# Performance work log

Hardware: AMD Instinct MI355X
Metric: run time of the kernel (lower is better)

## Reference

```python
import jax, jax.numpy as jnp
import numpy as np

DIM = 2048
MEM = 64
EPS = 1e-5


def setup_inputs() -> dict:
    key = jax.random.key(0)
    ks = jax.random.split(key, 6)
    x = jax.random.normal(ks[0], (8, 4096, DIM), dtype=jnp.float32)
    memory_slots = jax.random.normal(ks[1], (MEM, DIM), dtype=jnp.float32) * 0.02
    # memory_gate: Linear(dim -> memory_size)
    Wg = jax.random.normal(ks[2], (DIM, MEM), dtype=jnp.float32) / np.sqrt(DIM)
    bg = jnp.zeros((MEM,), dtype=jnp.float32)
    # memory_update: Linear(2*dim -> dim)
    Wu = jax.random.normal(ks[3], (2 * DIM, DIM), dtype=jnp.float32) / np.sqrt(2 * DIM)
    bu = jnp.zeros((DIM,), dtype=jnp.float32)
    gamma = jnp.ones((DIM,), dtype=jnp.float32)
    beta = jnp.zeros((DIM,), dtype=jnp.float32)
    return {"x": x, "memory_slots": memory_slots, "Wg": Wg, "bg": bg,
            "Wu": Wu, "bu": bu, "gamma": gamma, "beta": beta}


def _layer_norm(h, gamma, beta):
    mu = jnp.mean(h, axis=-1, keepdims=True)
    var = jnp.mean(jnp.square(h - mu), axis=-1, keepdims=True)
    return (h - mu) * jax.lax.rsqrt(var + EPS) * gamma + beta


def reference(x, memory_slots, Wg, bg, Wu, bu, gamma, beta):
    # gates: [B, S, M]
    memory_gates = jax.nn.sigmoid(jnp.einsum('bsd,dm->bsm', x, Wg) + bg)
    # retrieval: [B, S, D]
    memory_retrieved = jnp.einsum('bsm,md->bsd', memory_gates, memory_slots)
    combined = jnp.concatenate([x, memory_retrieved], axis=-1)  # [B, S, 2D]
    memory_enhanced = jnp.einsum('bse,ed->bsd', combined, Wu) + bu
    return _layer_norm(memory_enhanced, gamma, beta)
```

## Files before the change

### kernel.cpp

```cpp
#include <hip/hip_runtime.h>
#include <hip/hip_bf16.h>

typedef __bf16 bf16x8 __attribute__((ext_vector_type(8)));
typedef float f32x4 __attribute__((ext_vector_type(4)));
typedef float f32x16 __attribute__((ext_vector_type(16)));
typedef unsigned short u16;
typedef u16 u16x8 __attribute__((ext_vector_type(8)));

#define DIM 2048
#define MEM 64
#define KC 2112
#define MTOK 32768
#define BK 32
#define NT (KC/BK)

__device__ __forceinline__ u16 f2bf(float f) {
  union { float f; unsigned u; } v; v.f = f;
  unsigned r = v.u + 0x7FFF + ((v.u >> 16) & 1);
  return (u16)(r >> 16);
}
__device__ __forceinline__ float bf2f(u16 u) {
  union { unsigned u; float f; } v; v.u = ((unsigned)u) << 16; return v.f;
}

#define GLDS16(g, l) __builtin_amdgcn_global_load_lds( \
    (const __attribute__((address_space(1))) void*)(g), \
    (__attribute__((address_space(3))) void*)(l), 16, 0, 0)

__global__ __launch_bounds__(256) void prep_wu1(const float* __restrict__ Wu,
                                                u16* __restrict__ WcatT) {
  __shared__ float tile[64][65];
  int bk = blockIdx.x & 31;
  int bn = blockIdx.x >> 5;
  int tx = threadIdx.x & 63, g = threadIdx.x >> 6;
#pragma unroll
  for (int i = 0; i < 16; ++i)
    tile[g + i*4][tx] = Wu[(size_t)(bk*64 + g + i*4)*DIM + bn*64 + tx];
  __syncthreads();
#pragma unroll
  for (int i = 0; i < 16; ++i) {
    int n = bn*64 + g + i*4;
    WcatT[(size_t)n*KC + bk*64 + tx] = f2bf(tile[tx][g + i*4]);
  }
}

__global__ __launch_bounds__(256) void prep_m2a(const float* __restrict__ ms,
                                                const float* __restrict__ Wu,
                                                float* __restrict__ M2p) {
  int n  = blockIdx.x*256 + threadIdx.x;
  int mg = blockIdx.y;
  int kc = blockIdx.z;
  const float* w2 = Wu + (size_t)DIM*DIM + n;
  const float* m0 = ms + (size_t)(mg*4+0)*DIM;
  const float* m1 = ms + (size_t)(mg*4+1)*DIM;
  const float* m2 = ms + (size_t)(mg*4+2)*DIM;
  const float* m3 = ms + (size_t)(mg*4+3)*DIM;
  float a0=0.f, a1=0.f, a2=0.f, a3=0.f;
  int d0 = kc*256;
  for (int d = d0; d < d0+256; ++d) {
    float w = w2[(size_t)d*DIM];
    a0 += m0[d]*w; a1 += m1[d]*w; a2 += m2[d]*w; a3 += m3[d]*w;
  }
  M2p[((size_t)kc*64 + mg*4 + 0)*2048 + n] = a0;
  M2p[((size_t)kc*64 + mg*4 + 1)*2048 + n] = a1;
  M2p[((size_t)kc*64 + mg*4 + 2)*2048 + n] = a2;
  M2p[((size_t)kc*64 + mg*4 + 3)*2048 + n] = a3;
}

__global__ __launch_bounds__(256) void prep_m2b(const float* __restrict__ M2p,
                                                u16* __restrict__ WcatT) {
  int i = blockIdx.x*256 + threadIdx.x;
  float s = 0.f;
#pragma unroll
  for (int kc = 0; kc < 8; ++kc) s += M2p[(size_t)kc*131072 + i];
  int m = i >> 11, n = i & 2047;
  WcatT[(size_t)n*KC + DIM + m] = f2bf(s);
}

__global__ __launch_bounds__(256) void prep_wg(const float* __restrict__ Wg,
                                               u16* __restrict__ WgT) {
  __shared__ float tile[64][65];
  int k0 = blockIdx.x * 64;
  int tx = threadIdx.x & 63, g = threadIdx.x >> 6;
#pragma unroll
  for (int i = 0; i < 16; ++i)
    tile[g + i*4][tx] = Wg[(size_t)(k0 + g + i*4)*MEM + tx];
  __syncthreads();
#pragma unroll
  for (int i = 0; i < 16; ++i) {
    int m = g + i*4;
    WgT[(size_t)m*DIM + k0 + tx] = f2bf(tile[tx][m]);
  }
}

__global__ __launch_bounds__(256) void conv_gates(const float* __restrict__ x,
                                                  const u16* __restrict__ WgT,
                                                  const float* __restrict__ bg,
                                                  u16* __restrict__ Acat) {
  __shared__ u16 As[64*32];
  __shared__ u16 Bs[64*32];
  const int brow = blockIdx.x;
  const int tid = threadIdx.x;
  const int w = tid >> 6, l = tid & 63;
  const int wm = w >> 1, wn = w & 1;
  const int lrow = l & 15, lk = l >> 4;

  const int r  = tid >> 2;
  const int cb = (tid & 3) * 8;
  const float* xp = x + (size_t)(brow*64 + r)*DIM + cb;
  u16* aout = Acat + (size_t)(brow*64 + r)*KC + cb;

  f32x4 acc[2][2] = {};
  const bf16x8* Al = reinterpret_cast<const bf16x8*>(As);
  const bf16x8* Bl = reinterpret_cast<const bf16x8*>(Bs);
  const int abase = (wm*32 + lrow)*4 + lk;
  const int bbase = (wn*32 + lrow)*4 + lk;

  float4 v0 = *reinterpret_cast<const float4*>(xp);
  float4 v1 = *reinterpret_cast<const float4*>(xp + 4);

  for (int k0 = 0; k0 < DIM; k0 += 32) {
    const u16* bgp = WgT + (size_t)(tid>>2)*DIM + k0 + (tid&3)*8;
    GLDS16(bgp, ((u16*)Bs) + tid*8);
    u16x8 o;
    o[0]=f2bf(v0.x); o[1]=f2bf(v0.y); o[2]=f2bf(v0.z); o[3]=f2bf(v0.w);
    o[4]=f2bf(v1.x); o[5]=f2bf(v1.y); o[6]=f2bf(v1.z); o[7]=f2bf(v1.w);
    const bool more = (k0 + 32 < DIM);
    if (more) {
      v0 = *reinterpret_cast<const float4*>(xp + k0 + 32);
      v1 = *reinterpret_cast<const float4*>(xp + k0 + 36);
    }
    __builtin_amdgcn_s_barrier();
    *reinterpret_cast<u16x8*>(As + tid*8) = o;
    *reinterpret_cast<u16x8*>(aout + k0) = o;
    if (more) { asm volatile("s_waitcnt vmcnt(3) lgkmcnt(0)" ::: "memory"); }
    else      { asm volatile("s_waitcnt vmcnt(1) lgkmcnt(0)" ::: "memory"); }
    __builtin_amdgcn_sched_barrier(0);
    __builtin_amdgcn_s_barrier();
    bf16x8 a0v = Al[abase], a1v = Al[abase + 64];
    bf16x8 b0v = Bl[bbase], b1v = Bl[bbase + 64];
    acc[0][0] = __builtin_amdgcn_mfma_f32_16x16x32_bf16(a0v, b0v, acc[0][0], 0, 0, 0);
    acc[0][1] = __builtin_amdgcn_mfma_f32_16x16x32_bf16(a0v, b1v, acc[0][1], 0, 0, 0);
    acc[1][0] = __builtin_amdgcn_mfma_f32_16x16x32_bf16(a1v, b0v, acc[1][0], 0, 0, 0);
    acc[1][1] = __builtin_amdgcn_mfma_f32_16x16x32_bf16(a1v, b1v, acc[1][1], 0, 0, 0);
  }

#pragma unroll
  for (int fn = 0; fn < 2; ++fn) {
    int c = wn*32 + fn*16 + lrow;
    float b = bg[c];
#pragma unroll
    for (int fm = 0; fm < 2; ++fm)
#pragma unroll
      for (int rg = 0; rg < 4; ++rg) {
        int t = brow*64 + wm*32 + fm*16 + lk*4 + rg;
        float logit = acc[fm][fn][rg] + b;
        float gv = 1.0f / (1.0f + __expf(-logit));
        Acat[(size_t)t*KC + DIM + c] = f2bf(gv);
      }
  }
}

__global__ __launch_bounds__(512, 2) void gemm_main8(const u16* __restrict__ A,
                                                     const u16* __restrict__ Bt,
                                                     const float* __restrict__ bu,
                                                     float* __restrict__ Hf,
                                                     u16* __restrict__ Hb) {
  __shared__ u16 AsB[4*8192];
  __shared__ u16 BsB[4*8192];

  const int bid = blockIdx.x;
  const int wg  = (bid & 7) * (int)(gridDim.x >> 3) + (bid >> 3);
  const int brow = wg >> 3;
  const int bcol = wg & 7;
  const int tid = threadIdx.x;
  const int w = tid >> 6, l = tid & 63;
  const int wm = w >> 2, wn = w & 3;
  const int l31 = l & 31, lr5 = l >> 5;

  const int xor5  = ((tid >> 5) & 1) << 5;
  const int kelem = (((tid & 3) * 16) ^ xor5) >> 1;
  const int rowst = tid >> 2;
  const u16* Asrc0 = A  + (size_t)(brow*256 + rowst)*KC + kelem;
  const u16* Asrc1 = A  + (size_t)(brow*256 + 128 + rowst)*KC + kelem;
  const u16* Bsrc0 = Bt + (size_t)(bcol*256 + rowst)*KC + kelem;
  const u16* Bsrc1 = Bt + (size_t)(bcol*256 + 128 + rowst)*KC + kelem;
  const int p0 = tid*16, p1 = 8192 + tid*16;
  char* AsC = (char*)AsB;
  char* BsC = (char*)BsB;

  int aoff[4][2], boff[2][2];
#pragma unroll
  for (int rf = 0; rf < 4; ++rf)
#pragma unroll
    for (int ks = 0; ks < 2; ++ks) {
      int row = wm*128 + rf*32 + l31;
      int lg  = row*64 + ks*32 + lr5*16;
      aoff[rf][ks] = lg ^ (((row >> 3) & 1) << 5);
    }
#pragma unroll
  for (int cf = 0; cf < 2; ++cf)
#pragma unroll
    for (int ks = 0; ks < 2; ++ks) {
      int row = wn*64 + cf*32 + l31;
      int lg  = row*64 + ks*32 + lr5*16;
      boff[cf][ks] = lg ^ (((row >> 3) & 1) << 5);
    }

  f32x16 acc[4][2] = {};

#define STAGE_A(kt) { const int bb_ = ((kt)&3)*16384; \
    GLDS16(Asrc0 + (size_t)(kt)*BK, AsC + bb_ + p0); \
    GLDS16(Asrc1 + (size_t)(kt)*BK, AsC + bb_ + p1); }
#define STAGE_B(kt) { const int bb_ = ((kt)&3)*16384; \
    GLDS16(Bsrc0 + (size_t)(kt)*BK, BsC + bb_ + p0); \
    GLDS16(Bsrc1 + (size_t)(kt)*BK, BsC + bb_ + p1); }
#define MFMA32(av, bv, c) __builtin_amdgcn_mfma_f32_32x32x16_bf16(av, bv, c, 0, 0, 0)

  STAGE_A(0); STAGE_B(0);
  STAGE_A(1); STAGE_B(1);
  STAGE_A(2); STAGE_B(2);
  asm volatile("s_waitcnt vmcnt(8)" ::: "memory");
  __builtin_amdgcn_sched_barrier(0);
  __builtin_amdgcn_s_barrier();
  __builtin_amdgcn_sched_barrier(0);

#pragma unroll 1
  for (int t = 0; t < NT; ++t) {
    const char* Ab = AsC + (t & 3) * 16384;
    const char* Bb = BsC + (t & 3) * 16384;

    bf16x8 a0 = *(const bf16x8*)(Ab + aoff[0][0]);
    bf16x8 a1 = *(const bf16x8*)(Ab + aoff[1][0]);
    bf16x8 a2 = *(const bf16x8*)(Ab + aoff[2][0]);
    bf16x8 a3 = *(const bf16x8*)(Ab + aoff[3][0]);
    bf16x8 b0 = *(const bf16x8*)(Bb + boff[0][0]);
    bf16x8 b1 = *(const bf16x8*)(Bb + boff[1][0]);
    if (t + 3 < NT) STAGE_A(t + 3);
    __builtin_amdgcn_s_setprio(1);
    acc[0][0] = MFMA32(a0, b0, acc[0][0]);
    acc[0][1] = MFMA32(a0, b1, acc[0][1]);
    acc[1][0] = MFMA32(a1, b0, acc[1][0]);
    acc[1][1] = MFMA32(a1, b1, acc[1][1]);
    acc[2][0] = MFMA32(a2, b0, acc[2][0]);
    acc[2][1] = MFMA32(a2, b1, acc[2][1]);
    acc[3][0] = MFMA32(a3, b0, acc[3][0]);
    acc[3][1] = MFMA32(a3, b1, acc[3][1]);
    __builtin_amdgcn_s_setprio(0);

    bf16x8 a4 = *(const bf16x8*)(Ab + aoff[0][1]);
    bf16x8 a5 = *(const bf16x8*)(Ab + aoff[1][1]);
    bf16x8 a6 = *(const bf16x8*)(Ab + aoff[2][1]);
    bf16x8 a7 = *(const bf16x8*)(Ab + aoff[3][1]);
    bf16x8 b2 = *(const bf16x8*)(Bb + boff[0][1]);
    bf16x8 b3 = *(const bf16x8*)(Bb + boff[1][1]);
    if (t + 3 < NT) STAGE_B(t + 3);
    __builtin_amdgcn_s_setprio(1);
    acc[0][0] = MFMA32(a4, b2, acc[0][0]);
    acc[0][1] = MFMA32(a4, b3, acc[0][1]);
    acc[1][0] = MFMA32(a5, b2, acc[1][0]);
    acc[1][1] = MFMA32(a5, b3, acc[1][1]);
    acc[2][0] = MFMA32(a6, b2, acc[2][0]);
    acc[2][1] = MFMA32(a6, b3, acc[2][1]);
    acc[3][0] = MFMA32(a7, b2, acc[3][0]);
    acc[3][1] = MFMA32(a7, b3, acc[3][1]);
    __builtin_amdgcn_s_setprio(0);

    if (t <= NT-4)      { asm volatile("s_waitcnt vmcnt(8)" ::: "memory"); }
    else if (t == NT-3) { asm volatile("s_waitcnt vmcnt(4)" ::: "memory"); }
    else                { asm volatile("s_waitcnt vmcnt(0)" ::: "memory"); }
    __builtin_amdgcn_sched_barrier(0);
    __builtin_amdgcn_s_barrier();
    __builtin_amdgcn_sched_barrier(0);
  }
#undef STAGE_A
#undef STAGE_B
#undef MFMA32

  const int orow = brow*256 + wm*128;
  const int ocol = bcol*256 + wn*64;
  if (Hb) {
#pragma unroll
    for (int cf = 0; cf < 2; ++cf) {
      const int c = ocol + cf*32 + l31;
      const float bias = bu[c];
#pragma unroll
      for (int rf = 0; rf < 4; ++rf) {
        const int br = orow + rf*32 + 4*lr5;
#pragma unroll
        for (int reg = 0; reg < 16; ++reg) {
          const int row = br + (reg & 3) + 8*(reg >> 2);
          Hb[(size_t)row*DIM + c] = f2bf(acc[rf][cf][reg] + bias);
        }
      }
    }
  } else {
#pragma unroll
    for (int cf = 0; cf < 2; ++cf) {
      const int c = ocol + cf*32 + l31;
      const float bias = bu[c];
#pragma unroll
      for (int rf = 0; rf < 4; ++rf) {
        const int br = orow + rf*32 + 4*lr5;
#pragma unroll
        for (int reg = 0; reg < 16; ++reg) {
          const int row = br + (reg & 3) + 8*(reg >> 2);
          Hf[(size_t)row*DIM + c] = acc[rf][cf][reg] + bias;
        }
      }
    }
  }
}

__global__ __launch_bounds__(256) void ln_b(const u16* __restrict__ Hb,
                                            float* __restrict__ out,
                                            const float* __restrict__ gamma,
                                            const float* __restrict__ beta) {
  int row = blockIdx.x;
  const u16* h = Hb + (size_t)row*DIM;
  int tid = threadIdx.x;
  u16x8 hv = *reinterpret_cast<const u16x8*>(h + tid*8);
  float v[8];
#pragma unroll
  for (int j = 0; j < 8; ++j) v[j] = bf2f(hv[j]);
  float s = 0.f, s2 = 0.f;
#pragma unroll
  for (int j = 0; j < 8; ++j) { s += v[j]; s2 += v[j]*v[j]; }
#pragma unroll
  for (int o = 32; o >= 1; o >>= 1) { s += __shfl_xor(s, o); s2 += __shfl_xor(s2, o); }
  __shared__ float ss[4], ss2[4];
  int w = tid >> 6;
  if ((tid & 63) == 0) { ss[w] = s; ss2[w] = s2; }
  __syncthreads();
  s  = ss[0]+ss[1]+ss[2]+ss[3];
  s2 = ss2[0]+ss2[1]+ss2[2]+ss2[3];
  float mu  = s * (1.0f/DIM);
  float var = s2 * (1.0f/DIM) - mu*mu;
  float rs  = rsqrtf(var + 1e-5f);
  int c0 = tid*8;
  float o8[8];
#pragma unroll
  for (int j = 0; j < 8; ++j) o8[j] = (v[j]-mu)*rs*gamma[c0+j] + beta[c0+j];
  float4 oa = {o8[0],o8[1],o8[2],o8[3]}, ob = {o8[4],o8[5],o8[6],o8[7]};
  float* op = out + (size_t)row*DIM;
  reinterpret_cast<float4*>(op)[tid*2]   = oa;
  reinterpret_cast<float4*>(op)[tid*2+1] = ob;
}

__global__ __launch_bounds__(256) void ln_inplace(float* __restrict__ H,
                                                  const float* __restrict__ gamma,
                                                  const float* __restrict__ beta) {
  int row = blockIdx.x;
  float* h = H + (size_t)row*DIM;
  int tid = threadIdx.x;
  float4 a = reinterpret_cast<const float4*>(h)[tid*2];
  float4 b = reinterpret_cast<const float4*>(h)[tid*2+1];
  float v[8] = {a.x,a.y,a.z,a.w,b.x,b.y,b.z,b.w};
  float s = 0.f, s2 = 0.f;
#pragma unroll
  for (int j = 0; j < 8; ++j) { s += v[j]; s2 += v[j]*v[j]; }
#pragma unroll
  for (int o = 32; o >= 1; o >>= 1) { s += __shfl_xor(s, o); s2 += __shfl_xor(s2, o); }
  __shared__ float ss[4], ss2[4];
  int w = tid >> 6;
  if ((tid & 63) == 0) { ss[w] = s; ss2[w] = s2; }
  __syncthreads();
  s  = ss[0]+ss[1]+ss[2]+ss[3];
  s2 = ss2[0]+ss2[1]+ss2[2]+ss2[3];
  float mu  = s * (1.0f/DIM);
  float var = s2 * (1.0f/DIM) - mu*mu;
  float rs  = rsqrtf(var + 1e-5f);
  int c0 = tid*8;
  float o8[8];
#pragma unroll
  for (int j = 0; j < 8; ++j) o8[j] = (v[j]-mu)*rs*gamma[c0+j] + beta[c0+j];
  float4 oa = {o8[0],o8[1],o8[2],o8[3]}, ob = {o8[4],o8[5],o8[6],o8[7]};
  reinterpret_cast<float4*>(h)[tid*2]   = oa;
  reinterpret_cast<float4*>(h)[tid*2+1] = ob;
}

extern "C" void kernel_launch(void* const* d_in, const int* in_sizes, int n_in,
                              void* d_out, int out_size, void* d_ws, size_t ws_size,
                              hipStream_t stream) {
  const float* x     = (const float*)d_in[0];
  const float* ms    = (const float*)d_in[1];
  const float* Wg    = (const float*)d_in[2];
  const float* bg    = (const float*)d_in[3];
  const float* Wu    = (const float*)d_in[4];
  const float* bu    = (const float*)d_in[5];
  const float* gamma = (const float*)d_in[6];
  const float* beta  = (const float*)d_in[7];
  float* out = (float*)d_out;

  char* wsp = (char*)d_ws;
  const size_t offAcat  = 0;
  const size_t offWcatT = offAcat  + (size_t)MTOK*KC*2;
  const size_t offWgT   = offWcatT + (size_t)DIM*KC*2;
  const size_t offHb    = offWgT   + (size_t)MEM*DIM*2;
  const size_t needHb   = offHb + (size_t)MTOK*DIM*2;

  u16* Acat  = (u16*)(wsp + offAcat);
  u16* WcatT = (u16*)(wsp + offWcatT);
  u16* WgT   = (u16*)(wsp + offWgT);
  float* M2p = (float*)wsp;
  u16* Hb    = (ws_size >= needHb) ? (u16*)(wsp + offHb) : nullptr;

  prep_m2a<<<dim3(8,16,8), 256, 0, stream>>>(ms, Wu, M2p);
  prep_m2b<<<512, 256, 0, stream>>>(M2p, WcatT);
  prep_wu1<<<1024, 256, 0, stream>>>(Wu, WcatT);
  prep_wg<<<32, 256, 0, stream>>>(Wg, WgT);
  conv_gates<<<512, 256, 0, stream>>>(x, WgT, bg, Acat);
  gemm_main8<<<1024, 512, 0, stream>>>(Acat, WcatT, bu, out, Hb);
  if (Hb) ln_b<<<32768, 256, 0, stream>>>(Hb, out, gamma, beta);
  else    ln_inplace<<<32768, 256, 0, stream>>>(out, gamma, beta);
}
```

Before: 525.2 us.

## Process two K-tiles per barrier to halve workgroup synchronizations

The GEMM main loop now handles K-tiles in pairs. Loads for the next pair are issued during the first tile's phases, and a single vmcnt(0) wait plus barrier follows each pair instead of one barrier per tile. The prefetch depth changes from three tiles in flight to a two-tile lookahead, and the loop waits for all outstanding loads at each pair boundary. Fewer barriers cut sync overhead, but the full drain may expose more global-load latency.

Result: no change. 533.6 us (+1.6%).

```diff
diff --git a/kernel.cpp b/kernel.cpp
--- a/kernel.cpp
+++ b/kernel.cpp
@@ -216,63 +216,54 @@
     GLDS16(Bsrc0 + (size_t)(kt)*BK, BsC + bb_ + p0); \
     GLDS16(Bsrc1 + (size_t)(kt)*BK, BsC + bb_ + p1); }
 #define MFMA32(av, bv, c) __builtin_amdgcn_mfma_f32_32x32x16_bf16(av, bv, c, 0, 0, 0)
+#define PHASE(Ab_, Bb_, ks_, STG) { \
+    bf16x8 pa0 = *(const bf16x8*)((Ab_) + aoff[0][ks_]); \
+    bf16x8 pa1 = *(const bf16x8*)((Ab_) + aoff[1][ks_]); \
+    bf16x8 pa2 = *(const bf16x8*)((Ab_) + aoff[2][ks_]); \
+    bf16x8 pa3 = *(const bf16x8*)((Ab_) + aoff[3][ks_]); \
+    bf16x8 pb0 = *(const bf16x8*)((Bb_) + boff[0][ks_]); \
+    bf16x8 pb1 = *(const bf16x8*)((Bb_) + boff[1][ks_]); \
+    STG; \
+    __builtin_amdgcn_s_setprio(1); \
+    acc[0][0] = MFMA32(pa0, pb0, acc[0][0]); \
+    acc[0][1] = MFMA32(pa0, pb1, acc[0][1]); \
+    acc[1][0] = MFMA32(pa1, pb0, acc[1][0]); \
+    acc[1][1] = MFMA32(pa1, pb1, acc[1][1]); \
+    acc[2][0] = MFMA32(pa2, pb0, acc[2][0]); \
+    acc[2][1] = MFMA32(pa2, pb1, acc[2][1]); \
+    acc[3][0] = MFMA32(pa3, pb0, acc[3][0]); \
+    acc[3][1] = MFMA32(pa3, pb1, acc[3][1]); \
+    __builtin_amdgcn_s_setprio(0); }
 
   STAGE_A(0); STAGE_B(0);
   STAGE_A(1); STAGE_B(1);
-  STAGE_A(2); STAGE_B(2);
-  asm volatile("s_waitcnt vmcnt(8)" ::: "memory");
+  asm volatile("s_waitcnt vmcnt(0)" ::: "memory");
   __builtin_amdgcn_sched_barrier(0);
   __builtin_amdgcn_s_barrier();
   __builtin_amdgcn_sched_barrier(0);
 
 #pragma unroll 1
-  for (int t = 0; t < NT; ++t) {
-    const char* Ab = AsC + (t & 3) * 16384;
-    const char* Bb = BsC + (t & 3) * 16384;
-
-    bf16x8 a0 = *(const bf16x8*)(Ab + aoff[0][0]);
-    bf16x8 a1 = *(const bf16x8*)(Ab + aoff[1][0]);
-    bf16x8 a2 = *(const bf16x8*)(Ab + aoff[2][0]);
-    bf16x8 a3 = *(const bf16x8*)(Ab + aoff[3][0]);
-    bf16x8 b0 = *(const bf16x8*)(Bb + boff[0][0]);
-    bf16x8 b1 = *(const bf16x8*)(Bb + boff[1][0]);
-    if (t + 3 < NT) STAGE_A(t + 3);
-    __builtin_amdgcn_s_setprio(1);
-    acc[0][0] = MFMA32(a0, b0, acc[0][0]);
-    acc[0][1] = MFMA32(a0, b1, acc[0][1]);
-    acc[1][0] = MFMA32(a1, b0, acc[1][0]);
-    acc[1][1] = MFMA32(a1, b1, acc[1][1]);
-    acc[2][0] = MFMA32(a2, b0, acc[2][0]);
-    acc[2][1] = MFMA32(a2, b1, acc[2][1]);
-    acc[3][0] = MFMA32(a3, b0, acc[3][0]);
-    acc[3][1] = MFMA32(a3, b1, acc[3][1]);
-    __builtin_amdgcn_s_setprio(0);
-
-    bf16x8 a4 = *(const bf16x8*)(Ab + aoff[0][1]);
-    bf16x8 a5 = *(const bf16x8*)(Ab + aoff[1][1]);
-    bf16x8 a6 = *(const bf16x8*)(Ab + aoff[2][1]);
-    bf16x8 a7 = *(const bf16x8*)(Ab + aoff[3][1]);
-    bf16x8 b2 = *(const bf16x8*)(Bb + boff[0][1]);
-    bf16x8 b3 = *(const bf16x8*)(Bb + boff[1][1]);
-    if (t + 3 < NT) STAGE_B(t + 3);
-    __builtin_amdgcn_s_setprio(1);
-    acc[0][0] = MFMA32(a4, b2, acc[0][0]);
-    acc[0][1] = MFMA32(a4, b3, acc[0][1]);
-    acc[1][0] = MFMA32(a5, b2, acc[1][0]);
-    acc[1][1] = MFMA32(a5, b3, acc[1][1]);
-    acc[2][0] = MFMA32(a6, b2, acc[2][0]);
-    acc[2][1] = MFMA32(a6, b3, acc[2][1]);
-    acc[3][0] = MFMA32(a7, b2, acc[3][0]);
-    acc[3][1] = MFMA32(a7, b3, acc[3][1]);
-    __builtin_amdgcn_s_setprio(0);
-
-    if (t <= NT-4)      { asm volatile("s_waitcnt vmcnt(8)" ::: "memory"); }
-    else if (t == NT-3) { asm volatile("s_waitcnt vmcnt(4)" ::: "memory"); }
-    else                { asm volatile("s_waitcnt vmcnt(0)" ::: "memory"); }
-    __builtin_amdgcn_sched_barrier(0);
-    __builtin_amdgcn_s_barrier();
-    __builtin_amdgcn_sched_barrier(0);
-  }
+  for (int p = 0; p < NT/2; ++p) {
+    const int t0 = 2*p, t1 = 2*p + 1;
+    const char* Ab0 = AsC + (t0 & 3) * 16384;
+    const char* Bb0 = BsC + (t0 & 3) * 16384;
+    const char* Ab1 = AsC + (t1 & 3) * 16384;
+    const char* Bb1 = BsC + (t1 & 3) * 16384;
+    const bool more = (p + 1 < NT/2);
+
+    PHASE(Ab0, Bb0, 0, if (more) { STAGE_A(t0 + 2); STAGE_B(t0 + 2); })
+    PHASE(Ab0, Bb0, 1, if (more) { STAGE_A(t1 + 2); STAGE_B(t1 + 2); })
+    PHASE(Ab1, Bb1, 0, )
+    PHASE(Ab1, Bb1, 1, )
+
+    if (more) {
+      asm volatile("s_waitcnt vmcnt(0)" ::: "memory");
+      __builtin_amdgcn_sched_barrier(0);
+      __builtin_amdgcn_s_barrier();
+      __builtin_amdgcn_sched_barrier(0);
+    }
+  }
+#undef PHASE
 #undef STAGE_A
 #undef STAGE_B
 #undef MFMA32
```
